# Kernel tuning notes

Hardware: AMD Instinct MI355X
Metric: run time of the kernel (lower is better)

Reference implementation:

```python
import jax, jax.numpy as jnp
import numpy as np

N = 100000      # nodes
E = 1600000     # edges
G = 256         # graphs
NF = 2          # dataset.num_features
NC = 2          # dataset.num_classes
DIM = 32
BN_EPS = 1e-5


def _gin_layer(h, src, dst, w_in, b_in, w_out, b_out, gamma, beta):
    # GINConv (eps=0): h' = MLP(h + sum_{j in N(i)} h_j)
    agg = jax.ops.segment_sum(h[src], dst, num_segments=N)  # [N, d] scatter-add
    z = h + agg
    z = jax.nn.relu(z @ w_in + b_in) @ w_out + b_out        # 2-layer MLP
    z = jax.nn.relu(z)
    # BatchNorm1d (training-mode batch stats, biased var as in torch)
    mean = jnp.mean(z, axis=0)
    var = jnp.var(z, axis=0)
    return gamma * (z - mean) * jax.lax.rsqrt(var + BN_EPS) + beta


def setup_inputs() -> dict:
    key = jax.random.key(0)
    ks = jax.random.split(key, 20)
    s = 0.1
    x = jax.random.normal(ks[0], (N, NF), dtype=jnp.float32)
    edge_index = jax.random.randint(ks[1], (2, E), 0, N, dtype=jnp.int64)
    batch = jnp.sort(jax.random.randint(ks[2], (N,), 0, G, dtype=jnp.int64))
    return {
        "x": x,
        "edge_index": edge_index,
        "batch": batch,
        "w1_in": jax.random.normal(ks[3], (NF, DIM), dtype=jnp.float32) * s,
        "b1_in": jnp.zeros((DIM,), jnp.float32),
        "w1_out": jax.random.normal(ks[4], (DIM, DIM), dtype=jnp.float32) * s,
        "b1_out": jnp.zeros((DIM,), jnp.float32),
        "ws_in": jax.random.normal(ks[5], (4, DIM, DIM), dtype=jnp.float32) * s,
        "bs_in": jnp.zeros((4, DIM), jnp.float32),
        "ws_out": jax.random.normal(ks[6], (4, DIM, DIM), dtype=jnp.float32) * s,
        "bs_out": jnp.zeros((4, DIM), jnp.float32),
        "bn_gamma": jnp.ones((5, DIM), jnp.float32),
        "bn_beta": jnp.zeros((5, DIM), jnp.float32),
        "fc1_w": jax.random.normal(ks[7], (DIM, DIM), dtype=jnp.float32) * s,
        "fc1_b": jnp.zeros((DIM,), jnp.float32),
        "fc2_w": jax.random.normal(ks[8], (DIM, NC), dtype=jnp.float32) * s,
        "fc2_b": jnp.zeros((NC,), jnp.float32),
    }


def reference(x, edge_index, batch, w1_in, b1_in, w1_out, b1_out,
              ws_in, bs_in, ws_out, bs_out, bn_gamma, bn_beta,
              fc1_w, fc1_b, fc2_w, fc2_b):
    src, dst = edge_index[0], edge_index[1]
    h = _gin_layer(x, src, dst, w1_in, b1_in, w1_out, b1_out, bn_gamma[0], bn_beta[0])
    for i in range(4):  # convs 2..5 (structurally identical)
        h = _gin_layer(h, src, dst, ws_in[i], bs_in[i], ws_out[i], bs_out[i],
                       bn_gamma[i + 1], bn_beta[i + 1])
    g = jax.ops.segment_sum(h, batch, num_segments=G)  # global_add_pool -> [G, DIM]
    g = jax.nn.relu(g @ fc1_w + fc1_b)
    # dropout is identity in eval mode
    g = g @ fc2_w + fc2_b
    return jax.nn.log_softmax(g, axis=-1)
```

## Files before the change

### kernel.cpp

```cpp
#include <hip/hip_runtime.h>
#include <math.h>

#define NN 100000
#define NE 1600000
#define NG 256
#define NPART 200
#define PS 500
#define CAP 9000
#define EPB 2048
#define NBLK ((NE + EPB - 1) / EPB)
#define DEGB 64
static constexpr float BN_EPS = 1e-5f;

__device__ inline float h2f(unsigned short u) {
    _Float16 h; __builtin_memcpy(&h, &u, 2); return (float)h;
}
__device__ inline unsigned short f2h(float f) {
    _Float16 h = (_Float16)f; unsigned short u; __builtin_memcpy(&u, &h, 2); return u;
}
__device__ inline unsigned int pack2(float a, float b) {
    return (unsigned int)f2h(a) | ((unsigned int)f2h(b) << 16);
}

__global__ __launch_bounds__(256) void bucket_k(const int* __restrict__ src,
                                                const int* __restrict__ dst,
                                                int* __restrict__ bcur,
                                                unsigned int* __restrict__ bpk) {
    __shared__ int cnt[NPART];
    __shared__ int base[NPART];
    int t = threadIdx.x;
    for (int i = t; i < NPART; i += 256) cnt[i] = 0;
    __syncthreads();
    int eb = blockIdx.x * EPB + t * 8;
    bool act = eb < NE;
    int myp[8], myr[8];
    unsigned int pk[8];
    if (act) {
        int4 d0 = *reinterpret_cast<const int4*>(dst + eb);
        int4 d1 = *reinterpret_cast<const int4*>(dst + eb + 4);
        int4 s0 = *reinterpret_cast<const int4*>(src + eb);
        int4 s1 = *reinterpret_cast<const int4*>(src + eb + 4);
        int dd[8] = {d0.x,d0.y,d0.z,d0.w,d1.x,d1.y,d1.z,d1.w};
        int ss[8] = {s0.x,s0.y,s0.z,s0.w,s1.x,s1.y,s1.z,s1.w};
        #pragma unroll
        for (int i = 0; i < 8; i++) {
            int p = dd[i] / PS;
            myp[i] = p;
            pk[i] = ((unsigned int)ss[i] << 9) | (unsigned int)(dd[i] - p * PS);
            myr[i] = atomicAdd(&cnt[p], 1);
        }
    }
    __syncthreads();
    for (int i = t; i < NPART; i += 256)
        base[i] = cnt[i] ? atomicAdd(&bcur[i], cnt[i]) : 0;
    __syncthreads();
    if (act) {
        #pragma unroll
        for (int i = 0; i < 8; i++)
            bpk[myp[i] * CAP + base[myp[i]] + myr[i]] = pk[i];
    }
}

__global__ __launch_bounds__(256) void build_k(const int* __restrict__ bcur,
                                               const unsigned int* __restrict__ bpk,
                                               int* __restrict__ rowptr,
                                               int* __restrict__ csr,
                                               int* __restrict__ perm) {
    __shared__ int hist[PS];
    __shared__ int allc[NPART];
    __shared__ int psum[256];
    __shared__ int bc[DEGB];
    int p = blockIdx.x, t = threadIdx.x;
    int lo = p * PS;
    if (t < NPART) allc[t] = bcur[t];
    for (int i = t; i < PS; i += 256) hist[i] = 0;
    if (t < DEGB) bc[t] = 0;
    __syncthreads();
    int base = 0;
    for (int q = 0; q < p; q++) base += allc[q];
    int cnt = allc[p];
    const unsigned int* bp = bpk + p * CAP;
    const uint4* bp4 = reinterpret_cast<const uint4*>(bp);
    int n4 = cnt >> 2;
    for (int i = t; i < n4; i += 256) {
        uint4 v = bp4[i];
        atomicAdd(&hist[v.x & 511u], 1);
        atomicAdd(&hist[v.y & 511u], 1);
        atomicAdd(&hist[v.z & 511u], 1);
        atomicAdd(&hist[v.w & 511u], 1);
    }
    for (int i = 4 * n4 + t; i < cnt; i += 256) atomicAdd(&hist[bp[i] & 511u], 1);
    __syncthreads();
    int j0 = t * 2;
    int d0v = 0, d1v = 0, tsum = 0;
    if (j0 < PS) {
        d0v = hist[j0]; d1v = hist[j0 + 1];
        tsum = d0v + d1v;
        atomicAdd(&bc[d0v < DEGB ? d0v : DEGB - 1], 1);
        atomicAdd(&bc[d1v < DEGB ? d1v : DEGB - 1], 1);
    }
    psum[t] = tsum;
    __syncthreads();
    for (int off = 1; off < 256; off <<= 1) {
        int v = (t >= off) ? psum[t - off] : 0;
        __syncthreads();
        psum[t] += v;
        __syncthreads();
    }
    int texcl = psum[t] - tsum;
    if (j0 < PS) {
        int run = base + texcl;
        hist[j0] = run; rowptr[lo + j0] = run; run += d0v;
        hist[j0 + 1] = run; rowptr[lo + j0 + 1] = run; run += d1v;
    }
    if (p == NPART - 1 && t == 0) rowptr[NN] = base + cnt;
    __syncthreads();
    if (t == 0) {
        int run = 0;
        #pragma unroll
        for (int b = 0; b < DEGB; b++) { int c = bc[b]; bc[b] = run; run += c; }
    }
    __syncthreads();
    if (j0 < PS) {
        int r0 = atomicAdd(&bc[d0v < DEGB ? d0v : DEGB - 1], 1);
        perm[lo + r0] = lo + j0;
        int r1 = atomicAdd(&bc[d1v < DEGB ? d1v : DEGB - 1], 1);
        perm[lo + r1] = lo + j0 + 1;
    }
    __syncthreads();
    for (int i = t; i < n4; i += 256) {
        uint4 v = bp4[i];
        csr[atomicAdd(&hist[v.x & 511u], 1)] = v.x >> 9;
        csr[atomicAdd(&hist[v.y & 511u], 1)] = v.y >> 9;
        csr[atomicAdd(&hist[v.z & 511u], 1)] = v.z >> 9;
        csr[atomicAdd(&hist[v.w & 511u], 1)] = v.w >> 9;
    }
    for (int i = 4 * n4 + t; i < cnt; i += 256)
        csr[atomicAdd(&hist[bp[i] & 511u], 1)] = bp[i] >> 9;
}

__global__ __launch_bounds__(256) void gmlp1_k(
        const float* __restrict__ x, const int* __restrict__ perm,
        const int* __restrict__ rowptr, const int* __restrict__ csr,
        const float* __restrict__ w_in, const float* __restrict__ b_in,
        const float* __restrict__ w_out, const float* __restrict__ b_out,
        unsigned short* __restrict__ zout, float* __restrict__ stats) {
    __shared__ float lwi[64], lbi[32], lwo[1024], lbo[32];
    __shared__ float zin[128][33];
    int t = threadIdx.x;
    int n = t >> 1, q = t & 1, c0 = q * 16;
    for (int i = t; i < 1024; i += 256) lwo[i] = w_out[i];
    if (t < 64) lwi[t] = w_in[t];
    if (t < 32) { lbi[t] = b_in[t]; lbo[t] = b_out[t]; }
    __syncthreads();
    int gid = blockIdx.x * 128 + n;
    bool act = gid < NN;
    int node = act ? perm[gid] : 0;
    float h0 = 0.f, h1 = 0.f;
    if (act) {
        int rs = rowptr[node], re = rowptr[node + 1];
        if (q == 0) {
            float2 self = *reinterpret_cast<const float2*>(x + 2 * (size_t)node);
            h0 = self.x; h1 = self.y;
        }
        float g0 = 0.f, g1 = 0.f;
        int k = rs + q;
        for (; k + 6 < re; k += 8) {
            int s0 = csr[k], s1 = csr[k + 2], s2 = csr[k + 4], s3 = csr[k + 6];
            float2 v0 = *reinterpret_cast<const float2*>(x + 2 * (size_t)s0);
            float2 v1 = *reinterpret_cast<const float2*>(x + 2 * (size_t)s1);
            float2 v2 = *reinterpret_cast<const float2*>(x + 2 * (size_t)s2);
            float2 v3 = *reinterpret_cast<const float2*>(x + 2 * (size_t)s3);
            h0 += v0.x + v2.x; h1 += v0.y + v2.y;
            g0 += v1.x + v3.x; g1 += v1.y + v3.y;
        }
        for (; k < re; k += 2) {
            int s = csr[k];
            float2 v = *reinterpret_cast<const float2*>(x + 2 * (size_t)s);
            h0 += v.x; h1 += v.y;
        }
        h0 += g0; h1 += g1;
    }
    h0 += __shfl_xor(h0, 1);
    h1 += __shfl_xor(h1, 1);
    float y[16];
    #pragma unroll
    for (int j = 0; j < 16; j++) {
        float a = lbi[c0 + j] + h0 * lwi[c0 + j] + h1 * lwi[32 + c0 + j];
        y[j] = a > 0.f ? a : 0.f;
    }
    #pragma unroll
    for (int j = 0; j < 16; j++) zin[n][c0 + j] = act ? y[j] : 0.f;
    __syncthreads();
    float o[16];
    #pragma unroll
    for (int j = 0; j < 16; j++) o[j] = lbo[c0 + j];
    #pragma unroll
    for (int c = 0; c < 32; c++) {
        float yv = zin[n][c];
        #pragma unroll
        for (int j = 0; j < 16; j++) o[j] += yv * lwo[c * 32 + c0 + j];
    }
    #pragma unroll
    for (int j = 0; j < 16; j++) o[j] = o[j] > 0.f ? o[j] : 0.f;
    if (act) {
        unsigned short* zo = zout + (size_t)node * 32 + c0;
        uint4 wa, wb;
        wa.x = pack2(o[0], o[1]);   wa.y = pack2(o[2], o[3]);
        wa.z = pack2(o[4], o[5]);   wa.w = pack2(o[6], o[7]);
        wb.x = pack2(o[8], o[9]);   wb.y = pack2(o[10], o[11]);
        wb.z = pack2(o[12], o[13]); wb.w = pack2(o[14], o[15]);
        *reinterpret_cast<uint4*>(zo) = wa;
        *reinterpret_cast<uint4*>(zo + 8) = wb;
    }
    __syncthreads();
    #pragma unroll
    for (int j = 0; j < 16; j++) zin[n][c0 + j] = act ? o[j] : 0.f;
    __syncthreads();
    if (t < 32) {
        float s = 0.f, sq = 0.f;
        for (int nn = 0; nn < 128; nn++) {
            float v = zin[nn][t];
            s += v; sq += v * v;
        }
        atomicAdd(&stats[t], s);
        atomicAdd(&stats[32 + t], sq);
    }
}

__global__ __launch_bounds__(256) void gmlp32_k(
        const unsigned short* __restrict__ z, const int* __restrict__ perm,
        const float* __restrict__ statsIn,
        const float* __restrict__ gamma, const float* __restrict__ beta,
        const int* __restrict__ rowptr, const int* __restrict__ csr,
        const float* __restrict__ w_in, const float* __restrict__ b_in,
        const float* __restrict__ w_out, const float* __restrict__ b_out,
        unsigned short* __restrict__ zout, float* __restrict__ statsOut) {
    __shared__ float lwi[1024], lwo[1024], lbi[32], lbo[32], lsc[64];
    __shared__ float zin[128][33];
    int t = threadIdx.x;
    int n = t >> 1, q = t & 1, c0 = q * 16;
    for (int i = t; i < 1024; i += 256) { lwi[i] = w_in[i]; lwo[i] = w_out[i]; }
    if (t < 32) {
        lbi[t] = b_in[t]; lbo[t] = b_out[t];
        float mean = statsIn[t] * (1.f / NN);
        float var  = statsIn[32 + t] * (1.f / NN) - mean * mean;
        float scale = gamma[t] * rsqrtf(var + BN_EPS);
        lsc[t] = scale;
        lsc[32 + t] = beta[t] - mean * scale;
    }
    __syncthreads();
    int gid = blockIdx.x * 128 + n;
    bool act = gid < NN;
    int node = act ? perm[gid] : 0;
    float a[16];
    #pragma unroll
    for (int j = 0; j < 16; j++) a[j] = 0.f;
    float cntf = 0.f;
    if (act) {
        int rs = rowptr[node], re = rowptr[node + 1];
        cntf = (float)(re - rs + 1);
        const unsigned short* zb = z + (size_t)node * 32 + c0;
        uint4 sa = *reinterpret_cast<const uint4*>(zb);
        uint4 sb = *reinterpret_cast<const uint4*>(zb + 8);
        const unsigned short* pa = reinterpret_cast<const unsigned short*>(&sa);
        const unsigned short* pb = reinterpret_cast<const unsigned short*>(&sb);
        #pragma unroll
        for (int j = 0; j < 8; j++) { a[j] = h2f(pa[j]); a[8 + j] = h2f(pb[j]); }
        int k = rs;
        for (; k + 4 <= re; k += 4) {
            int s0 = csr[k], s1 = csr[k + 1], s2 = csr[k + 2], s3 = csr[k + 3];
            const unsigned short* r0 = z + (size_t)s0 * 32 + c0;
            const unsigned short* r1 = z + (size_t)s1 * 32 + c0;
            const unsigned short* r2 = z + (size_t)s2 * 32 + c0;
            const unsigned short* r3 = z + (size_t)s3 * 32 + c0;
            uint4 v0a = *reinterpret_cast<const uint4*>(r0);
            uint4 v0b = *reinterpret_cast<const uint4*>(r0 + 8);
            uint4 v1a = *reinterpret_cast<const uint4*>(r1);
            uint4 v1b = *reinterpret_cast<const uint4*>(r1 + 8);
            uint4 v2a = *reinterpret_cast<const uint4*>(r2);
            uint4 v2b = *reinterpret_cast<const uint4*>(r2 + 8);
            uint4 v3a = *reinterpret_cast<const uint4*>(r3);
            uint4 v3b = *reinterpret_cast<const uint4*>(r3 + 8);
            const unsigned short* q0a = reinterpret_cast<const unsigned short*>(&v0a);
            const unsigned short* q0b = reinterpret_cast<const unsigned short*>(&v0b);
            const unsigned short* q1a = reinterpret_cast<const unsigned short*>(&v1a);
            const unsigned short* q1b = reinterpret_cast<const unsigned short*>(&v1b);
            const unsigned short* q2a = reinterpret_cast<const unsigned short*>(&v2a);
            const unsigned short* q2b = reinterpret_cast<const unsigned short*>(&v2b);
            const unsigned short* q3a = reinterpret_cast<const unsigned short*>(&v3a);
            const unsigned short* q3b = reinterpret_cast<const unsigned short*>(&v3b);
            #pragma unroll
            for (int j = 0; j < 8; j++) {
                a[j]     += (h2f(q0a[j]) + h2f(q1a[j])) + (h2f(q2a[j]) + h2f(q3a[j]));
                a[8 + j] += (h2f(q0b[j]) + h2f(q1b[j])) + (h2f(q2b[j]) + h2f(q3b[j]));
            }
        }
        for (; k < re; k++) {
            int s = csr[k];
            const unsigned short* r = z + (size_t)s * 32 + c0;
            uint4 va = *reinterpret_cast<const uint4*>(r);
            uint4 vb = *reinterpret_cast<const uint4*>(r + 8);
            const unsigned short* qa = reinterpret_cast<const unsigned short*>(&va);
            const unsigned short* qb = reinterpret_cast<const unsigned short*>(&vb);
            #pragma unroll
            for (int j = 0; j < 8; j++) { a[j] += h2f(qa[j]); a[8 + j] += h2f(qb[j]); }
        }
    }
    #pragma unroll
    for (int j = 0; j < 16; j++)
        zin[n][c0 + j] = act ? (a[j] * lsc[c0 + j] + cntf * lsc[32 + c0 + j]) : 0.f;
    __syncthreads();
    float y[16];
    #pragma unroll
    for (int j = 0; j < 16; j++) y[j] = lbi[c0 + j];
    #pragma unroll
    for (int c = 0; c < 32; c++) {
        float zv = zin[n][c];
        #pragma unroll
        for (int j = 0; j < 16; j++) y[j] += zv * lwi[c * 32 + c0 + j];
    }
    #pragma unroll
    for (int j = 0; j < 16; j++) y[j] = y[j] > 0.f ? y[j] : 0.f;
    __syncthreads();
    #pragma unroll
    for (int j = 0; j < 16; j++) zin[n][c0 + j] = y[j];
    __syncthreads();
    float o[16];
    #pragma unroll
    for (int j = 0; j < 16; j++) o[j] = lbo[c0 + j];
    #pragma unroll
    for (int c = 0; c < 32; c++) {
        float yv = zin[n][c];
        #pragma unroll
        for (int j = 0; j < 16; j++) o[j] += yv * lwo[c * 32 + c0 + j];
    }
    #pragma unroll
    for (int j = 0; j < 16; j++) o[j] = o[j] > 0.f ? o[j] : 0.f;
    if (act) {
        unsigned short* zo = zout + (size_t)node * 32 + c0;
        uint4 wa, wb;
        wa.x = pack2(o[0], o[1]);   wa.y = pack2(o[2], o[3]);
        wa.z = pack2(o[4], o[5]);   wa.w = pack2(o[6], o[7]);
        wb.x = pack2(o[8], o[9]);   wb.y = pack2(o[10], o[11]);
        wb.z = pack2(o[12], o[13]); wb.w = pack2(o[14], o[15]);
        *reinterpret_cast<uint4*>(zo) = wa;
        *reinterpret_cast<uint4*>(zo + 8) = wb;
    }
    __syncthreads();
    #pragma unroll
    for (int j = 0; j < 16; j++) zin[n][c0 + j] = act ? o[j] : 0.f;
    __syncthreads();
    if (t < 32) {
        float s = 0.f, sq = 0.f;
        for (int nn = 0; nn < 128; nn++) {
            float v = zin[nn][t];
            s += v; sq += v * v;
        }
        atomicAdd(&statsOut[t], s);
        atomicAdd(&statsOut[32 + t], sq);
    }
}

__global__ __launch_bounds__(256) void pool_seg_k(
        const unsigned short* __restrict__ z,
        const float* __restrict__ statsIn,
        const float* __restrict__ gamma, const float* __restrict__ beta,
        const int* __restrict__ batch, float* __restrict__ g) {
    __shared__ float lsc[64];
    __shared__ float part[32][33];
    int t = threadIdx.x, slot = t >> 3, q = t & 7, c0 = q * 4;
    int gr = blockIdx.x;
    if (t < 32) {
        float mean = statsIn[t] * (1.f / NN);
        float var  = statsIn[32 + t] * (1.f / NN) - mean * mean;
        float scale = gamma[t] * rsqrtf(var + BN_EPS);
        lsc[t] = scale;
        lsc[32 + t] = beta[t] - mean * scale;
    }
    int lo = 0, hi = NN;
    while (lo < hi) { int mid = (lo + hi) >> 1; if (batch[mid] < gr) lo = mid + 1; else hi = mid; }
    int start = lo;
    hi = NN;
    while (lo < hi) { int mid = (lo + hi) >> 1; if (batch[mid] < gr + 1) lo = mid + 1; else hi = mid; }
    int end = lo;
    float a0 = 0.f, a1 = 0.f, a2 = 0.f, a3 = 0.f;
    for (int i = start + slot; i < end; i += 32) {
        ushort4 v = *reinterpret_cast<const ushort4*>(z + (size_t)i * 32 + c0);
        a0 += h2f(v.x); a1 += h2f(v.y); a2 += h2f(v.z); a3 += h2f(v.w);
    }
    part[slot][c0+0] = a0; part[slot][c0+1] = a1;
    part[slot][c0+2] = a2; part[slot][c0+3] = a3;
    __syncthreads();
    if (t < 32) {
        float s = 0.f;
        for (int sl = 0; sl < 32; sl++) s += part[sl][t];
        float cnt = (float)(end - start);
        g[(size_t)gr * 32 + t] = s * lsc[t] + cnt * lsc[32 + t];
    }
}

__global__ __launch_bounds__(256) void head_k(
        const float* __restrict__ g,
        const float* __restrict__ fc1w, const float* __restrict__ fc1b,
        const float* __restrict__ fc2w, const float* __restrict__ fc2b,
        float* __restrict__ out) {
    __shared__ float lw1[1024], lb1[32], lw2[64], lb2[2];
    int t = threadIdx.x;
    for (int i = t; i < 1024; i += 256) lw1[i] = fc1w[i];
    if (t < 32) lb1[t] = fc1b[t];
    if (t < 64) lw2[t] = fc2w[t];
    if (t < 2) lb2[t] = fc2b[t];
    __syncthreads();
    float gv[32];
    #pragma unroll
    for (int c = 0; c < 32; c++) gv[c] = g[(size_t)t * 32 + c];
    float o0 = lb2[0], o1 = lb2[1];
    #pragma unroll 4
    for (int k = 0; k < 32; k++) {
        float a = lb1[k];
        #pragma unroll
        for (int c = 0; c < 32; c++) a += gv[c] * lw1[c * 32 + k];
        a = a > 0.f ? a : 0.f;
        o0 += a * lw2[k * 2 + 0];
        o1 += a * lw2[k * 2 + 1];
    }
    float m = fmaxf(o0, o1);
    float lse = m + logf(expf(o0 - m) + expf(o1 - m));
    out[t * 2 + 0] = o0 - lse;
    out[t * 2 + 1] = o1 - lse;
}

extern "C" void kernel_launch(void* const* d_in, const int* in_sizes, int n_in,
                              void* d_out, int out_size, void* d_ws, size_t ws_size,
                              hipStream_t stream) {
    const float* x      = (const float*)d_in[0];
    const int*   ei     = (const int*)d_in[1];
    const int*   src    = ei;
    const int*   dst    = ei + NE;
    const int*   batch  = (const int*)d_in[2];
    const float* w1_in  = (const float*)d_in[3];
    const float* b1_in  = (const float*)d_in[4];
    const float* w1_out = (const float*)d_in[5];
    const float* b1_out = (const float*)d_in[6];
    const float* ws_in  = (const float*)d_in[7];
    const float* bs_in  = (const float*)d_in[8];
    const float* ws_out = (const float*)d_in[9];
    const float* bs_out = (const float*)d_in[10];
    const float* gamma  = (const float*)d_in[11];
    const float* beta   = (const float*)d_in[12];
    const float* fc1w   = (const float*)d_in[13];
    const float* fc1b   = (const float*)d_in[14];
    const float* fc2w   = (const float*)d_in[15];
    const float* fc2b   = (const float*)d_in[16];
    float* out = (float*)d_out;

    unsigned short* bufA = (unsigned short*)d_ws;
    unsigned short* bufB = bufA + (size_t)NN * 32;
    float* stats  = (float*)(bufB + (size_t)NN * 32);
    int*   bcur   = (int*)(stats + 5 * 64);
    float* g      = (float*)(bcur + NPART);
    int*   perm   = (int*)(g + (size_t)NG * 32);
    int*   rowptr = perm + NN;
    int*   csr    = rowptr + NN + 4;
    unsigned int* bpk = (unsigned int*)(csr + NE);

    hipMemsetAsync(stats, 0, (size_t)(5 * 64 + NPART) * sizeof(int), stream);

    bucket_k<<<NBLK, 256, 0, stream>>>(src, dst, bcur, bpk);
    build_k<<<NPART, 256, 0, stream>>>(bcur, bpk, rowptr, csr, perm);

    gmlp1_k<<<(NN + 127) / 128, 256, 0, stream>>>(x, perm, rowptr, csr,
                                                  w1_in, b1_in, w1_out, b1_out, bufA, stats);

    const unsigned short* cur = bufA;
    unsigned short* nxt = bufB;
    for (int j = 0; j < 4; j++) {
        gmlp32_k<<<(NN + 127) / 128, 256, 0, stream>>>(cur, perm, stats + j * 64,
                                              gamma + j * 32, beta + j * 32,
                                              rowptr, csr,
                                              ws_in + j * 1024, bs_in + j * 32,
                                              ws_out + j * 1024, bs_out + j * 32,
                                              nxt, stats + (j + 1) * 64);
        unsigned short* tmp = (unsigned short*)cur; cur = nxt; nxt = tmp;
    }

    pool_seg_k<<<NG, 256, 0, stream>>>(cur, stats + 4 * 64,
                                       gamma + 4 * 32, beta + 4 * 32, batch, g);
    head_k<<<1, 256, 0, stream>>>(g, fc1w, fc1b, fc2w, fc2b, out);
}
```

Measured before the change: 389.4 us.

## Split features into column halves and gather each half in a separate pass

Node features are stored as two planar fp16 buffers of 16 channels each, so each neighbour row is 32 bytes instead of 64. Each layer's fused gather+MLP kernel is split into two gather passes, one per half, that write fp32 aggregates, followed by a separate MLP kernel. The intent is to shrink the gather working set so each half-table (3.2 MB) fits better in cache and random neighbour reads hit more often. In exchange it adds two extra launches per layer, reads the CSR twice, and writes and rereads fp32 aggregate buffers.

```diff
diff --git a/kernel.cpp b/kernel.cpp
--- a/kernel.cpp
+++ b/kernel.cpp
@@ -144,7 +144,8 @@
         const int* __restrict__ rowptr, const int* __restrict__ csr,
         const float* __restrict__ w_in, const float* __restrict__ b_in,
         const float* __restrict__ w_out, const float* __restrict__ b_out,
-        unsigned short* __restrict__ zout, float* __restrict__ stats) {
+        unsigned short* __restrict__ zlo, unsigned short* __restrict__ zhi,
+        float* __restrict__ stats) {
     __shared__ float lwi[64], lbi[32], lwo[1024], lbo[32];
     __shared__ float zin[128][33];
     int t = threadIdx.x;
@@ -204,7 +205,7 @@
     #pragma unroll
     for (int j = 0; j < 16; j++) o[j] = o[j] > 0.f ? o[j] : 0.f;
     if (act) {
-        unsigned short* zo = zout + (size_t)node * 32 + c0;
+        unsigned short* zo = (q ? zhi : zlo) + (size_t)node * 16;
         uint4 wa, wb;
         wa.x = pack2(o[0], o[1]);   wa.y = pack2(o[2], o[3]);
         wa.z = pack2(o[4], o[5]);   wa.w = pack2(o[6], o[7]);
@@ -228,14 +229,60 @@
     }
 }
 
-__global__ __launch_bounds__(256) void gmlp32_k(
-        const unsigned short* __restrict__ z, const int* __restrict__ perm,
+__global__ __launch_bounds__(256) void gather_k(
+        const unsigned short* __restrict__ zh, const int* __restrict__ perm,
+        const int* __restrict__ rowptr, const int* __restrict__ csr,
+        float* __restrict__ agg) {
+    int t = threadIdx.x;
+    int n = t >> 1, q = t & 1, c0 = q * 8;
+    int gid = blockIdx.x * 128 + n;
+    if (gid >= NN) return;
+    int node = perm[gid];
+    int rs = rowptr[node], re = rowptr[node + 1];
+    float a[8], b[8];
+    #pragma unroll
+    for (int j = 0; j < 8; j++) { a[j] = 0.f; b[j] = 0.f; }
+    int k = rs;
+    for (; k + 4 <= re; k += 4) {
+        int s0 = csr[k], s1 = csr[k + 1], s2 = csr[k + 2], s3 = csr[k + 3];
+        uint4 v0 = *reinterpret_cast<const uint4*>(zh + (size_t)s0 * 16 + c0);
+        uint4 v1 = *reinterpret_cast<const uint4*>(zh + (size_t)s1 * 16 + c0);
+        uint4 v2 = *reinterpret_cast<const uint4*>(zh + (size_t)s2 * 16 + c0);
+        uint4 v3 = *reinterpret_cast<const uint4*>(zh + (size_t)s3 * 16 + c0);
+        const unsigned short* p0 = reinterpret_cast<const unsigned short*>(&v0);
+        const unsigned short* p1 = reinterpret_cast<const unsigned short*>(&v1);
+        const unsigned short* p2 = reinterpret_cast<const unsigned short*>(&v2);
+        const unsigned short* p3 = reinterpret_cast<const unsigned short*>(&v3);
+        #pragma unroll
+        for (int j = 0; j < 8; j++) {
+            a[j] += h2f(p0[j]) + h2f(p2[j]);
+            b[j] += h2f(p1[j]) + h2f(p3[j]);
+        }
+    }
+    for (; k < re; k++) {
+        int s = csr[k];
+        uint4 v = *reinterpret_cast<const uint4*>(zh + (size_t)s * 16 + c0);
+        const unsigned short* pp = reinterpret_cast<const unsigned short*>(&v);
+        #pragma unroll
+        for (int j = 0; j < 8; j++) a[j] += h2f(pp[j]);
+    }
+    #pragma unroll
+    for (int j = 0; j < 8; j++) a[j] += b[j];
+    float* ap = agg + (size_t)node * 16 + c0;
+    *reinterpret_cast<float4*>(ap) = make_float4(a[0], a[1], a[2], a[3]);
+    *reinterpret_cast<float4*>(ap + 4) = make_float4(a[4], a[5], a[6], a[7]);
+}
+
+__global__ __launch_bounds__(256) void mlp_k(
+        const unsigned short* __restrict__ zlo, const unsigned short* __restrict__ zhi,
+        const float* __restrict__ agglo, const float* __restrict__ agghi,
+        const int* __restrict__ rowptr,
         const float* __restrict__ statsIn,
         const float* __restrict__ gamma, const float* __restrict__ beta,
-        const int* __restrict__ rowptr, const int* __restrict__ csr,
         const float* __restrict__ w_in, const float* __restrict__ b_in,
         const float* __restrict__ w_out, const float* __restrict__ b_out,
-        unsigned short* __restrict__ zout, float* __restrict__ statsOut) {
+        unsigned short* __restrict__ zloO, unsigned short* __restrict__ zhiO,
+        float* __restrict__ statsOut) {
     __shared__ float lwi[1024], lwo[1024], lbi[32], lbo[32], lsc[64];
     __shared__ float zin[128][33];
     int t = threadIdx.x;
@@ -250,66 +297,37 @@
         lsc[32 + t] = beta[t] - mean * scale;
     }
     __syncthreads();
-    int gid = blockIdx.x * 128 + n;
-    bool act = gid < NN;
-    int node = act ? perm[gid] : 0;
-    float a[16];
-    #pragma unroll
-    for (int j = 0; j < 16; j++) a[j] = 0.f;
+    int node = blockIdx.x * 128 + n;
+    bool act = node < NN;
+    float v[16];
     float cntf = 0.f;
     if (act) {
-        int rs = rowptr[node], re = rowptr[node + 1];
-        cntf = (float)(re - rs + 1);
-        const unsigned short* zb = z + (size_t)node * 32 + c0;
-        uint4 sa = *reinterpret_cast<const uint4*>(zb);
-        uint4 sb = *reinterpret_cast<const uint4*>(zb + 8);
+        const unsigned short* zs = (q ? zhi : zlo) + (size_t)node * 16;
+        uint4 sa = *reinterpret_cast<const uint4*>(zs);
+        uint4 sb = *reinterpret_cast<const uint4*>(zs + 8);
         const unsigned short* pa = reinterpret_cast<const unsigned short*>(&sa);
         const unsigned short* pb = reinterpret_cast<const unsigned short*>(&sb);
-        #pragma unroll
-        for (int j = 0; j < 8; j++) { a[j] = h2f(pa[j]); a[8 + j] = h2f(pb[j]); }
-        int k = rs;
-        for (; k + 4 <= re; k += 4) {
-            int s0 = csr[k], s1 = csr[k + 1], s2 = csr[k + 2], s3 = csr[k + 3];
-            const unsigned short* r0 = z + (size_t)s0 * 32 + c0;
-            const unsigned short* r1 = z + (size_t)s1 * 32 + c0;
-            const unsigned short* r2 = z + (size_t)s2 * 32 + c0;
-            const unsigned short* r3 = z + (size_t)s3 * 32 + c0;
-            uint4 v0a = *reinterpret_cast<const uint4*>(r0);
-            uint4 v0b = *reinterpret_cast<const uint4*>(r0 + 8);
-            uint4 v1a = *reinterpret_cast<const uint4*>(r1);
-            uint4 v1b = *reinterpret_cast<const uint4*>(r1 + 8);
-            uint4 v2a = *reinterpret_cast<const uint4*>(r2);
-            uint4 v2b = *reinterpret_cast<const uint4*>(r2 + 8);
-            uint4 v3a = *reinterpret_cast<const uint4*>(r3);
-            uint4 v3b = *reinterpret_cast<const uint4*>(r3 + 8);
-            const unsigned short* q0a = reinterpret_cast<const unsigned short*>(&v0a);
-            const unsigned short* q0b = reinterpret_cast<const unsigned short*>(&v0b);
-            const unsigned short* q1a = reinterpret_cast<const unsigned short*>(&v1a);
-            const unsigned short* q1b = reinterpret_cast<const unsigned short*>(&v1b);
-            const unsigned short* q2a = reinterpret_cast<const unsigned short*>(&v2a);
-            const unsigned short* q2b = reinterpret_cast<const unsigned short*>(&v2b);
-            const unsigned short* q3a = reinterpret_cast<const unsigned short*>(&v3a);
-            const unsigned short* q3b = reinterpret_cast<const unsigned short*>(&v3b);
-            #pragma unroll
-            for (int j = 0; j < 8; j++) {
-                a[j]     += (h2f(q0a[j]) + h2f(q1a[j])) + (h2f(q2a[j]) + h2f(q3a[j]));
-                a[8 + j] += (h2f(q0b[j]) + h2f(q1b[j])) + (h2f(q2b[j]) + h2f(q3b[j]));
-            }
-        }
-        for (; k < re; k++) {
-            int s = csr[k];
-            const unsigned short* r = z + (size_t)s * 32 + c0;
-            uint4 va = *reinterpret_cast<const uint4*>(r);
-            uint4 vb = *reinterpret_cast<const uint4*>(r + 8);
-            const unsigned short* qa = reinterpret_cast<const unsigned short*>(&va);
-            const unsigned short* qb = reinterpret_cast<const unsigned short*>(&vb);
-            #pragma unroll
-            for (int j = 0; j < 8; j++) { a[j] += h2f(qa[j]); a[8 + j] += h2f(qb[j]); }
-        }
+        const float* ag = (q ? agghi : agglo) + (size_t)node * 16;
+        float4 a0 = *reinterpret_cast<const float4*>(ag);
+        float4 a1 = *reinterpret_cast<const float4*>(ag + 4);
+        float4 a2 = *reinterpret_cast<const float4*>(ag + 8);
+        float4 a3 = *reinterpret_cast<const float4*>(ag + 12);
+        v[0] = h2f(pa[0]) + a0.x; v[1] = h2f(pa[1]) + a0.y;
+        v[2] = h2f(pa[2]) + a0.z; v[3] = h2f(pa[3]) + a0.w;
+        v[4] = h2f(pa[4]) + a1.x; v[5] = h2f(pa[5]) + a1.y;
+        v[6] = h2f(pa[6]) + a1.z; v[7] = h2f(pa[7]) + a1.w;
+        v[8]  = h2f(pb[0]) + a2.x; v[9]  = h2f(pb[1]) + a2.y;
+        v[10] = h2f(pb[2]) + a2.z; v[11] = h2f(pb[3]) + a2.w;
+        v[12] = h2f(pb[4]) + a3.x; v[13] = h2f(pb[5]) + a3.y;
+        v[14] = h2f(pb[6]) + a3.z; v[15] = h2f(pb[7]) + a3.w;
+        cntf = (float)(rowptr[node + 1] - rowptr[node] + 1);
+    } else {
+        #pragma unroll
+        for (int j = 0; j < 16; j++) v[j] = 0.f;
     }
     #pragma unroll
     for (int j = 0; j < 16; j++)
-        zin[n][c0 + j] = act ? (a[j] * lsc[c0 + j] + cntf * lsc[32 + c0 + j]) : 0.f;
+        zin[n][c0 + j] = act ? (v[j] * lsc[c0 + j] + cntf * lsc[32 + c0 + j]) : 0.f;
     __syncthreads();
     float y[16];
     #pragma unroll
@@ -338,7 +356,7 @@
     #pragma unroll
     for (int j = 0; j < 16; j++) o[j] = o[j] > 0.f ? o[j] : 0.f;
     if (act) {
-        unsigned short* zo = zout + (size_t)node * 32 + c0;
+        unsigned short* zo = (q ? zhiO : zloO) + (size_t)node * 16;
         uint4 wa, wb;
         wa.x = pack2(o[0], o[1]);   wa.y = pack2(o[2], o[3]);
         wa.z = pack2(o[4], o[5]);   wa.w = pack2(o[6], o[7]);
@@ -354,8 +372,8 @@
     if (t < 32) {
         float s = 0.f, sq = 0.f;
         for (int nn = 0; nn < 128; nn++) {
-            float v = zin[nn][t];
-            s += v; sq += v * v;
+            float vv = zin[nn][t];
+            s += vv; sq += vv * vv;
         }
         atomicAdd(&statsOut[t], s);
         atomicAdd(&statsOut[32 + t], sq);
@@ -363,7 +381,7 @@
 }
 
 __global__ __launch_bounds__(256) void pool_seg_k(
-        const unsigned short* __restrict__ z,
+        const unsigned short* __restrict__ zlo, const unsigned short* __restrict__ zhi,
         const float* __restrict__ statsIn,
         const float* __restrict__ gamma, const float* __restrict__ beta,
         const int* __restrict__ batch, float* __restrict__ g) {
@@ -384,9 +402,11 @@
     hi = NN;
     while (lo < hi) { int mid = (lo + hi) >> 1; if (batch[mid] < gr + 1) lo = mid + 1; else hi = mid; }
     int end = lo;
+    const unsigned short* zb = (c0 < 16) ? zlo : zhi;
+    int coff = (c0 < 16) ? c0 : (c0 - 16);
     float a0 = 0.f, a1 = 0.f, a2 = 0.f, a3 = 0.f;
     for (int i = start + slot; i < end; i += 32) {
-        ushort4 v = *reinterpret_cast<const ushort4*>(z + (size_t)i * 32 + c0);
+        ushort4 v = *reinterpret_cast<const ushort4*>(zb + (size_t)i * 16 + coff);
         a0 += h2f(v.x); a1 += h2f(v.y); a2 += h2f(v.z); a3 += h2f(v.w);
     }
     part[slot][c0+0] = a0; part[slot][c0+1] = a1;
@@ -455,9 +475,13 @@
     const float* fc2b   = (const float*)d_in[16];
     float* out = (float*)d_out;
 
-    unsigned short* bufA = (unsigned short*)d_ws;
-    unsigned short* bufB = bufA + (size_t)NN * 32;
-    float* stats  = (float*)(bufB + (size_t)NN * 32);
+    unsigned short* zloA = (unsigned short*)d_ws;
+    unsigned short* zhiA = zloA + (size_t)NN * 16;
+    unsigned short* zloB = zhiA + (size_t)NN * 16;
+    unsigned short* zhiB = zloB + (size_t)NN * 16;
+    float* agglo  = (float*)(zhiB + (size_t)NN * 16);
+    float* agghi  = agglo + (size_t)NN * 16;
+    float* stats  = agghi + (size_t)NN * 16;
     int*   bcur   = (int*)(stats + 5 * 64);
     float* g      = (float*)(bcur + NPART);
     int*   perm   = (int*)(g + (size_t)NG * 32);
@@ -471,21 +495,24 @@
     build_k<<<NPART, 256, 0, stream>>>(bcur, bpk, rowptr, csr, perm);
 
     gmlp1_k<<<(NN + 127) / 128, 256, 0, stream>>>(x, perm, rowptr, csr,
-                                                  w1_in, b1_in, w1_out, b1_out, bufA, stats);
-
-    const unsigned short* cur = bufA;
-    unsigned short* nxt = bufB;
+                                                  w1_in, b1_in, w1_out, b1_out,
+                                                  zloA, zhiA, stats);
+
+    unsigned short *clo = zloA, *chi = zhiA, *nlo = zloB, *nhi = zhiB;
     for (int j = 0; j < 4; j++) {
-        gmlp32_k<<<(NN + 127) / 128, 256, 0, stream>>>(cur, perm, stats + j * 64,
-                                              gamma + j * 32, beta + j * 32,
-                                              rowptr, csr,
-                                              ws_in + j * 1024, bs_in + j * 32,
-                                              ws_out + j * 1024, bs_out + j * 32,
-                                              nxt, stats + (j + 1) * 64);
-        unsigned short* tmp = (unsigned short*)cur; cur = nxt; nxt = tmp;
-    }
-
-    pool_seg_k<<<NG, 256, 0, stream>>>(cur, stats + 4 * 64,
+        gather_k<<<(NN + 127) / 128, 256, 0, stream>>>(clo, perm, rowptr, csr, agglo);
+        gather_k<<<(NN + 127) / 128, 256, 0, stream>>>(chi, perm, rowptr, csr, agghi);
+        mlp_k<<<(NN + 127) / 128, 256, 0, stream>>>(clo, chi, agglo, agghi, rowptr,
+                                                    stats + j * 64,
+                                                    gamma + j * 32, beta + j * 32,
+                                                    ws_in + j * 1024, bs_in + j * 32,
+                                                    ws_out + j * 1024, bs_out + j * 32,
+                                                    nlo, nhi, stats + (j + 1) * 64);
+        unsigned short* tl = clo; clo = nlo; nlo = tl;
+        unsigned short* th = chi; chi = nhi; nhi = th;
+    }
+
+    pool_seg_k<<<NG, 256, 0, stream>>>(clo, chi, stats + 4 * 64,
                                        gamma + 4 * 32, beta + 4 * 32, batch, g);
     head_k<<<1, 256, 0, stream>>>(g, fc1w, fc1b, fc2w, fc2b, out);
 }
```

Measured after the change: 469.8 us. 20.7% more time.
